# Kernel tuning notes

Measured on AMD Instinct MI355X. Metric: run time of the kernel, lower is better.

## Reference

```python
import jax, jax.numpy as jnp
import numpy as np

N_HEAD = 16
D_QK = 128
D_V = 128
D_MODEL = 2048
BATCH = 2
SEQ = 2048


def alibi_slopes(n_head):
    # standard ALiBi slopes: 2^(-8*i/n_head) for i = 1..n_head
    return jnp.asarray(2.0 ** (-8.0 * np.arange(1, n_head + 1) / n_head), dtype=jnp.float32)


def setup_inputs() -> dict:
    key = jax.random.key(0)
    k1, k2, k3, k4, k5 = jax.random.split(key, 5)
    x = jax.random.normal(k1, (BATCH, SEQ, D_MODEL), dtype=jnp.float32)
    # causal attention mask (1 = keep, 0 = masked), broadcast over heads
    causal = jnp.tril(jnp.ones((SEQ, SEQ), dtype=bool))
    attention_mask = jnp.broadcast_to(causal, (BATCH, 1, SEQ, SEQ))
    Wq = jax.random.normal(k2, (D_MODEL, N_HEAD * D_QK), dtype=jnp.float32) * (D_MODEL ** -0.5)
    Wk = jax.random.normal(k3, (D_MODEL, N_HEAD * D_QK), dtype=jnp.float32) * (D_MODEL ** -0.5)
    Wv = jax.random.normal(k4, (D_MODEL, N_HEAD * D_V), dtype=jnp.float32) * (D_MODEL ** -0.5)
    Wo = jax.random.normal(k5, (N_HEAD * D_V, D_MODEL), dtype=jnp.float32) * ((N_HEAD * D_V) ** -0.5)
    return {"x": x, "attention_mask": attention_mask, "Wq": Wq, "Wk": Wk, "Wv": Wv, "Wo": Wo}


def reference(x, attention_mask, Wq, Wk, Wv, Wo):
    B, S, _ = x.shape
    scale = D_QK ** -0.5
    q = (x @ Wq).reshape(B, S, N_HEAD, D_QK).transpose(0, 2, 1, 3)  # [B,H,S,dqk]
    k = (x @ Wk).reshape(B, S, N_HEAD, D_QK).transpose(0, 2, 1, 3)
    v = (x @ Wv).reshape(B, S, N_HEAD, D_V).transpose(0, 2, 1, 3)
    scores = jnp.einsum('bhid,bhjd->bhij', q, k) * scale  # [B,H,S,S]
    # ALiBi bias: slope_h * (j - i), negative penalty for distant past keys
    pos = jnp.arange(S, dtype=jnp.float32)
    rel = pos[None, :] - pos[:, None]  # [S,S]
    slopes = alibi_slopes(N_HEAD)
    scores = scores + slopes[None, :, None, None] * rel[None, None, :, :]
    scores = jnp.where(attention_mask, scores, jnp.float32(-jnp.inf))
    attn = jax.nn.softmax(scores, axis=-1)
    out = jnp.einsum('bhij,bhjd->bhid', attn, v)  # [B,H,S,dv]
    out = out.transpose(0, 2, 1, 3).reshape(B, S, N_HEAD * D_V)
    return out @ Wo
```

## Files before the change

### kernel.cpp

```cpp
#include <hip/hip_runtime.h>
#include <cstdint>

typedef unsigned short u16;
typedef __attribute__((ext_vector_type(4))) u16 u16x4;
typedef __attribute__((ext_vector_type(8))) u16 u16x8;
typedef __attribute__((ext_vector_type(8))) __bf16 bf16x8;
typedef __attribute__((ext_vector_type(4))) float f32x4;

#define LOG2E 1.44269504088896340736f

static __device__ __forceinline__ u16 f2bf(float f) {
  unsigned u = __builtin_bit_cast(unsigned, f);
  u += 0x7fffu + ((u >> 16) & 1u);
  return (u16)(u >> 16);
}
static __device__ __forceinline__ float bf2f(u16 v) {
  unsigned u = ((unsigned)v) << 16;
  return __builtin_bit_cast(float, u);
}

static __device__ __forceinline__ void gload16(const u16* g, u16* l) {
  __builtin_amdgcn_global_load_lds(
      (__attribute__((address_space(1))) void*)(uintptr_t)g,
      (__attribute__((address_space(3))) void*)(uintptr_t)l, 16, 0, 0);
}

static __device__ __forceinline__ bf16x8 lds_bf8(const void* p) {
  return __builtin_bit_cast(bf16x8, *(const u16x8*)p);
}

__global__ __launch_bounds__(256) void cast_x_kernel(const float* __restrict__ src,
                                                     u16* __restrict__ dst) {
  int i = (blockIdx.x * 256 + threadIdx.x) * 4;
  float4 v = *(const float4*)(src + i);
  u16x4 r = {f2bf(v.x), f2bf(v.y), f2bf(v.z), f2bf(v.w)};
  *(u16x4*)(dst + i) = r;
}

__device__ __forceinline__ void transpose_body(const float* __restrict__ src,
                                               u16* __restrict__ dst) {
  __shared__ float tile[32][33];
  const int n0 = blockIdx.x * 32, k0 = blockIdx.y * 32;
  const int tx = threadIdx.x & 31, ty = threadIdx.x >> 5;
#pragma unroll
  for (int r = 0; r < 4; ++r) {
    int row = r * 8 + ty;
    tile[row][tx] = src[(size_t)(k0 + row) * 2048 + n0 + tx];
  }
  __syncthreads();
#pragma unroll
  for (int r = 0; r < 4; ++r) {
    int row = r * 8 + ty;
    dst[(size_t)(n0 + row) * 2048 + k0 + tx] = f2bf(tile[tx][row]);
  }
}

__global__ __launch_bounds__(256) void transpose_w_kernel(const float* __restrict__ src,
                                                          u16* __restrict__ dst) {
  transpose_body(src, dst);
}

__global__ __launch_bounds__(256) void transpose_w3_kernel(const float* Wq, const float* Wk,
                                                           const float* Wv, u16* Wqt, u16* Wkt,
                                                           u16* Wvt) {
  const float* src = blockIdx.z == 0 ? Wq : (blockIdx.z == 1 ? Wk : Wv);
  u16* dst = blockIdx.z == 0 ? Wqt : (blockIdx.z == 1 ? Wkt : Wvt);
  transpose_body(src, dst);
}

#define GSTAGE(TILE, KH, BUF)                                                        \
  do {                                                                               \
    const int bk = (TILE) * 64 + (KH) * 32;                                          \
    u16* as_ = &lds[((BUF) * 2 + (KH)) * 8192];                                      \
    u16* bs_ = &lds[32768 + ((BUF) * 2 + (KH)) * BSLOT];                             \
    gload16(&A[(size_t)(m0 + sr) * 2048 + bk + scu], as_ + tid * 8);                 \
    gload16(&A[(size_t)(m0 + 128 + sr) * 2048 + bk + scu], as_ + 4096 + tid * 8);    \
    gload16(&Bt[(size_t)(n0 + sr) * 2048 + bk + scu], bs_ + tid * 8);                \
    if constexpr (BN == 256)                                                         \
      gload16(&Bt[(size_t)(n0 + 128 + sr) * 2048 + bk + scu], bs_ + 4096 + tid * 8); \
  } while (0)

#define GPH(BUF, KH, STAGE_STMT, VMLIT)                                              \
  do {                                                                               \
    const u16* as_ = &lds[((BUF) * 2 + (KH)) * 8192];                                \
    const u16* bs_ = &lds[32768 + ((BUF) * 2 + (KH)) * BSLOT];                       \
    bf16x8 af[8], bq[NF];                                                            \
    _Pragma("unroll") for (int mf = 0; mf < 8; ++mf) {                               \
      const int ar = wm * 128 + mf * 16 + l16;                                       \
      af[mf] = lds_bf8(&as_[(ar * 32 + lg * 8) ^ xsw]);                              \
    }                                                                                \
    _Pragma("unroll") for (int nf = 0; nf < NF; ++nf) {                              \
      const int br = wn * (BN / 4) + nf * 16 + l16;                                  \
      bq[nf] = lds_bf8(&bs_[(br * 32 + lg * 8) ^ xsw]);                              \
    }                                                                                \
    STAGE_STMT;                                                                      \
    asm volatile("s_barrier" ::: "memory");                                          \
    __builtin_amdgcn_s_setprio(1);                                                   \
    _Pragma("unroll") for (int mf = 0; mf < 8; ++mf)                                 \
        _Pragma("unroll") for (int nf = 0; nf < NF; ++nf) acc[mf][nf] =              \
            __builtin_amdgcn_mfma_f32_16x16x32_bf16(af[mf], bq[nf], acc[mf][nf], 0, 0, 0); \
    __builtin_amdgcn_s_setprio(0);                                                   \
    __builtin_amdgcn_sched_barrier(0);                                               \
    asm volatile("s_waitcnt vmcnt(" #VMLIT ")\n\ts_barrier" ::: "memory");           \
  } while (0)

template <int BN, int MODE>
__device__ __forceinline__ void gemm_dp(const u16* __restrict__ A, const u16* __restrict__ Bt,
                                        void* __restrict__ Cout, int m0, int n0) {
  constexpr int BSLOT = BN * 32;
  constexpr int NF = BN / 64;
  __shared__ u16 lds[32768 + 4 * BSLOT];
  const int tid = threadIdx.x, lane = tid & 63, w = tid >> 6;
  const int wm = w >> 2, wn = w & 3;
  const int l16 = lane & 15, lg = lane >> 4;
  const int sr = tid >> 2;
  const int scu = (((tid & 3) ^ ((tid >> 2) & 3))) * 8;
  const int xsw = (l16 & 3) * 8;

  f32x4 acc[8][NF];
#pragma unroll
  for (int i = 0; i < 8; ++i)
#pragma unroll
    for (int j = 0; j < NF; ++j) acc[i][j] = f32x4{0.f, 0.f, 0.f, 0.f};

  GSTAGE(0, 0, 0);
  GSTAGE(0, 1, 0);
  GSTAGE(1, 0, 1);
  if constexpr (BN == 256) {
    asm volatile("s_waitcnt vmcnt(8)\n\ts_barrier" ::: "memory");
    for (int m2 = 0; m2 < 30; m2 += 2) {
      GPH(0, 0, GSTAGE(m2 + 1, 1, 1), 8);
      GPH(0, 1, GSTAGE(m2 + 2, 0, 0), 8);
      GPH(1, 0, GSTAGE(m2 + 2, 1, 0), 8);
      GPH(1, 1, GSTAGE(m2 + 3, 0, 1), 8);
    }
    GPH(0, 0, GSTAGE(31, 1, 1), 8);
    GPH(0, 1, (void)0, 4);
    GPH(1, 0, (void)0, 0);
    GPH(1, 1, (void)0, 0);
  } else {
    asm volatile("s_waitcnt vmcnt(6)\n\ts_barrier" ::: "memory");
    for (int m2 = 0; m2 < 30; m2 += 2) {
      GPH(0, 0, GSTAGE(m2 + 1, 1, 1), 6);
      GPH(0, 1, GSTAGE(m2 + 2, 0, 0), 6);
      GPH(1, 0, GSTAGE(m2 + 2, 1, 0), 6);
      GPH(1, 1, GSTAGE(m2 + 3, 0, 1), 6);
    }
    GPH(0, 0, GSTAGE(31, 1, 1), 6);
    GPH(0, 1, (void)0, 3);
    GPH(1, 0, (void)0, 0);
    GPH(1, 1, (void)0, 0);
  }

  constexpr int WNS = BN / 4;
#pragma unroll
  for (int mf = 0; mf < 8; ++mf)
#pragma unroll
    for (int nf = 0; nf < NF; ++nf)
#pragma unroll
      for (int r = 0; r < 4; ++r) {
        const int row = m0 + wm * 128 + mf * 16 + lg * 4 + r;
        const int col = n0 + wn * WNS + nf * 16 + l16;
        const float v = acc[mf][nf][r];
        if constexpr (MODE == 0) {
          size_t off =
              (((size_t)(row >> 11) * 16 + (col >> 7)) * 2048 + (row & 2047)) * 128 + (col & 127);
          ((u16*)Cout)[off] = f2bf(v);
        } else if constexpr (MODE == 2) {
          size_t off =
              (((size_t)(col >> 11) * 16 + (row >> 7)) * 128 + (row & 127)) * 2048 + (col & 2047);
          ((u16*)Cout)[off] = f2bf(v);
        } else {
          ((float*)Cout)[(size_t)row * 2048 + col] = v;
        }
      }
}

__global__ __launch_bounds__(512, 2) void qkproj_kernel(const u16* xb, const u16* Wqt,
                                                        const u16* Wkt, u16* Qb, u16* Kb) {
  const int n0g = blockIdx.y * 256;
  const u16* Bt = (n0g < 2048) ? Wqt : Wkt;
  u16* dst = (n0g < 2048) ? Qb : Kb;
  gemm_dp<256, 0>(xb, Bt, dst, blockIdx.x * 256, n0g & 2047);
}

__global__ __launch_bounds__(512, 2) void vt_kernel(const u16* Wvt, const u16* xb, u16* Vb) {
  gemm_dp<128, 2>(Wvt, xb, Vb, blockIdx.x * 256, blockIdx.y * 128);
}

__global__ __launch_bounds__(512, 2) void out_kernel(const u16* OA, const u16* Wot, float* C) {
  gemm_dp<128, 1>(OA, Wot, C, blockIdx.x * 256, blockIdx.y * 128);
}

__global__ __launch_bounds__(256) void attn_kernel(const u16* __restrict__ Q,
                                                   const u16* __restrict__ Kg,
                                                   const u16* __restrict__ Vg,
                                                   u16* __restrict__ O,
                                                   u16* __restrict__ Opart,
                                                   float* __restrict__ Lp) {
  const int tid = threadIdx.x, lane = tid & 63, w = tid >> 6;
  const int l16 = lane & 15, lg = lane >> 4;

  const int bid = blockIdx.x;
  const int bh = bid / 23, u = bid - bh * 23;
  int tile, st0, st1, slot = 0;
  bool multi;
  if (u < 14) {
    multi = true;
    const int ti = u >> 1, ch = u & 1;
    tile = 9 + ti;
    const int s = 2 * tile + 2;
    st0 = ch * 18;
    st1 = min(st0 + 18, s);
    slot = bh * 14 + u;
  } else {
    multi = false;
    tile = 22 - u;
    st0 = 0;
    st1 = 2 * tile + 2;
  }
  const int q0 = tile * 128;
  const int h = bh & 15, b = bh >> 4;
  const float sl2 = exp2f(-0.5f * (float)(h + 1)) * LOG2E;
  const float sc2 = 0.08838834764831845f * LOG2E;

  __shared__ u16 Kl[64 * 128];
  __shared__ u16 Vl[128 * 64];
  __shared__ u16 Pl[128 * 64];

  const size_t qk_base = (size_t)bh * 2048 * 128;
  const size_t v_base = (size_t)bh * 128 * 2048;

  bf16x8 qf[2][4];
#pragma unroll
  for (int mf = 0; mf < 2; ++mf)
#pragma unroll
    for (int ks = 0; ks < 4; ++ks)
      qf[mf][ks] =
          lds_bf8(&Q[qk_base + (size_t)(q0 + w * 32 + mf * 16 + l16) * 128 + ks * 32 + lg * 8]);

  f32x4 oacc[2][8];
#pragma unroll
  for (int i = 0; i < 2; ++i)
#pragma unroll
    for (int j = 0; j < 8; ++j) oacc[i][j] = f32x4{0.f, 0.f, 0.f, 0.f};
  float lsum[2][2];
  lsum[0][0] = lsum[0][1] = lsum[1][0] = lsum[1][1] = 0.f;

  float ab[2][4][4];
#pragma unroll
  for (int mf = 0; mf < 2; ++mf)
#pragma unroll
    for (int nf = 0; nf < 4; ++nf)
#pragma unroll
      for (int r = 0; r < 4; ++r)
        ab[mf][nf][r] =
            (float)(st0 * 64 + nf * 16 + lg * 4 + r - q0 - w * 32 - mf * 16 - l16) * sl2;
  const float abinc = 64.0f * sl2;

  const u16* kgp = Kg + qk_base + (size_t)(tid >> 4) * 128 + (tid & 15) * 8;
  const u16* vgp = Vg + v_base + (size_t)(tid >> 3) * 2048 + (tid & 7) * 8;
  const int kwo = ((tid >> 4) * 256 + (tid & 15) * 16) ^ (((tid >> 4) & 7) << 4);
  const int vwo = ((tid >> 3) * 128 + (tid & 7) * 16) ^ (((tid >> 3) & 7) << 4);

  u16x8 kr[4], vr[4];
#define LOADREGS(STX)                                                        \
  do {                                                                       \
    const size_t ko = (size_t)(STX)*8192, vo = (size_t)(STX)*64;             \
    _Pragma("unroll") for (int s = 0; s < 4; ++s) {                          \
      kr[s] = *(const u16x8*)(kgp + ko + s * 2048);                          \
      vr[s] = *(const u16x8*)(vgp + vo + s * 65536);                         \
    }                                                                        \
  } while (0)

#define WRITEBUF()                                                           \
  do {                                                                       \
    _Pragma("unroll") for (int s = 0; s < 4; ++s) {                          \
      *(u16x8*)((char*)Kl + s * 4096 + kwo) = kr[s];                         \
      *(u16x8*)((char*)Vl + s * 4096 + vwo) = vr[s];                         \
    }                                                                        \
  } while (0)

#define ASTEP(MASKED)                                                                     \
  do {                                                                                    \
    if (st + 1 < st1) LOADREGS(st + 1);                                                   \
    f32x4 sacc[2][4];                                                                     \
    _Pragma("unroll") for (int i = 0; i < 2; ++i)                                         \
        _Pragma("unroll") for (int j = 0; j < 4; ++j) sacc[i][j] = f32x4{0.f, 0.f, 0.f, 0.f}; \
    __builtin_amdgcn_s_setprio(1);                                                        \
    _Pragma("unroll") for (int ks = 0; ks < 4; ++ks) {                                    \
      bf16x8 kf[4];                                                                       \
      _Pragma("unroll") for (int nf = 0; nf < 4; ++nf) {                                  \
        int j = nf * 16 + l16;                                                            \
        kf[nf] = lds_bf8((char*)Kl + ((j * 256 + (ks * 32 + lg * 8) * 2) ^ ((j & 7) << 4))); \
      }                                                                                   \
      _Pragma("unroll") for (int mf = 0; mf < 2; ++mf)                                    \
          _Pragma("unroll") for (int nf = 0; nf < 4; ++nf) sacc[mf][nf] =                 \
              __builtin_amdgcn_mfma_f32_16x16x32_bf16(kf[nf], qf[mf][ks], sacc[mf][nf], 0, 0, 0); \
    }                                                                                     \
    __builtin_amdgcn_s_setprio(0);                                                        \
    _Pragma("unroll") for (int mf = 0; mf < 2; ++mf)                                      \
        _Pragma("unroll") for (int nf = 0; nf < 4; ++nf) {                                \
      float pvv[4];                                                                       \
      _Pragma("unroll") for (int r = 0; r < 4; ++r) {                                     \
        float s2 = fmaf(sacc[mf][nf][r], sc2, ab[mf][nf][r]);                             \
        float pv = exp2f(s2);                                                             \
        if (MASKED) {                                                                     \
          const int rel = st * 64 + nf * 16 + lg * 4 + r - q0 - w * 32 - mf * 16 - l16;   \
          pv = (rel <= 0) ? pv : 0.f;                                                     \
        }                                                                                 \
        pvv[r] = pv;                                                                      \
        ab[mf][nf][r] += abinc;                                                           \
      }                                                                                   \
      lsum[mf][nf & 1] += (pvv[0] + pvv[1]) + (pvv[2] + pvv[3]);                          \
      unsigned w0_, w1_;                                                                  \
      asm("v_cvt_pk_bf16_f32 %0, %1, %2" : "=v"(w0_) : "v"(pvv[0]), "v"(pvv[1]));         \
      asm("v_cvt_pk_bf16_f32 %0, %1, %2" : "=v"(w1_) : "v"(pvv[2]), "v"(pvv[3]));         \
      const int qrow = w * 32 + mf * 16 + l16;                                            \
      uint2 pw_{w0_, w1_};                                                                \
      *(uint2*)((char*)Pl + ((qrow * 128 + (nf * 16 + lg * 4) * 2) ^ ((qrow & 7) << 4))) = pw_; \
    }                                                                                     \
    __builtin_amdgcn_s_setprio(1);                                                        \
    _Pragma("unroll") for (int ks = 0; ks < 2; ++ks) {                                    \
      bf16x8 pf[2];                                                                       \
      _Pragma("unroll") for (int mf = 0; mf < 2; ++mf) {                                  \
        int qrow = w * 32 + mf * 16 + l16;                                                \
        pf[mf] = lds_bf8((char*)Pl + ((qrow * 128 + (ks * 32 + lg * 8) * 2) ^ ((qrow & 7) << 4))); \
      }                                                                                   \
      _Pragma("unroll") for (int nf = 0; nf < 8; ++nf) {                                  \
        int d = nf * 16 + l16;                                                            \
        bf16x8 vf =                                                                       \
            lds_bf8((char*)Vl + ((d * 128 + (ks * 32 + lg * 8) * 2) ^ ((d & 7) << 4)));   \
        _Pragma("unroll") for (int mf = 0; mf < 2; ++mf) oacc[mf][nf] =                   \
            __builtin_amdgcn_mfma_f32_16x16x32_bf16(pf[mf], vf, oacc[mf][nf], 0, 0, 0);   \
      }                                                                                   \
    }                                                                                     \
    __builtin_amdgcn_s_setprio(0);                                                        \
    if (st + 1 < st1) {                                                                   \
      __syncthreads();                                                                    \
      WRITEBUF();                                                                         \
      __syncthreads();                                                                    \
    }                                                                                     \
  } while (0)

  LOADREGS(st0);
  WRITEBUF();
  __syncthreads();

  const int dstart = (multi && (u & 1) == 0) ? st1 : st1 - 2;
  int st = st0;
  for (; st < dstart; ++st) ASTEP(false);
  for (; st < st1; ++st) ASTEP(true);
#undef LOADREGS
#undef WRITEBUF
#undef ASTEP

  float lr[2];
#pragma unroll
  for (int mf = 0; mf < 2; ++mf) {
    float v = lsum[mf][0] + lsum[mf][1];
    v += __shfl_xor(v, 16, 64);
    v += __shfl_xor(v, 32, 64);
    lr[mf] = v;
  }

  if (multi) {
    if (lg == 0) {
#pragma unroll
      for (int mf = 0; mf < 2; ++mf) Lp[(size_t)slot * 128 + w * 32 + mf * 16 + l16] = lr[mf];
    }
#pragma unroll
    for (int mf = 0; mf < 2; ++mf)
#pragma unroll
      for (int r = 0; r < 4; ++r) {
        const int row = w * 32 + mf * 16 + lg * 4 + r;
#pragma unroll
        for (int nf = 0; nf < 8; ++nf) {
          int col = nf * 16 + l16;
          Opart[((size_t)slot * 128 + row) * 128 + col] = f2bf(oacc[mf][nf][r]);
        }
      }
  } else {
#pragma unroll
    for (int mf = 0; mf < 2; ++mf)
#pragma unroll
      for (int r = 0; r < 4; ++r) {
        const float lv = __shfl(lr[mf], lg * 4 + r, 64);
        const float inv = 1.0f / lv;
        const int srow = q0 + w * 32 + mf * 16 + lg * 4 + r;
#pragma unroll
        for (int nf = 0; nf < 8; ++nf) {
          int col = h * 128 + nf * 16 + l16;
          O[((size_t)b * 2048 + srow) * 2048 + col] = f2bf(oacc[mf][nf][r] * inv);
        }
      }
  }
}

__global__ __launch_bounds__(256) void combine_kernel(const u16* __restrict__ Opart,
                                                      const float* __restrict__ Lp,
                                                      u16* __restrict__ O) {
  const int bx = blockIdx.x;
  const int bh = bx / 7, ti = bx % 7;
  const int tile = 9 + ti;
  const int slot0 = bh * 14 + ti * 2, slot1 = slot0 + 1;
  const int b = bh >> 4, h = bh & 15;
  const int q0 = tile * 128;
  const int tid = threadIdx.x;
  const int colg = (tid & 15) * 8, rowb = tid >> 4;
#pragma unroll
  for (int rr = 0; rr < 8; ++rr) {
    const int row = rowb + rr * 16;
    const float l0 = Lp[(size_t)slot0 * 128 + row];
    const float l1 = Lp[(size_t)slot1 * 128 + row];
    const float inv = 1.0f / (l0 + l1);
    u16x8 p0 = *(const u16x8*)&Opart[((size_t)slot0 * 128 + row) * 128 + colg];
    u16x8 p1 = *(const u16x8*)&Opart[((size_t)slot1 * 128 + row) * 128 + colg];
    u16x8 o;
#pragma unroll
    for (int e = 0; e < 8; ++e) o[e] = f2bf((bf2f(p0[e]) + bf2f(p1[e])) * inv);
    *(u16x8*)&O[((size_t)b * 2048 + q0 + row) * 2048 + h * 128 + colg] = o;
  }
}

extern "C" void kernel_launch(void* const* d_in, const int* in_sizes, int n_in, void* d_out,
                              int out_size, void* d_ws, size_t ws_size, hipStream_t stream) {
  const float* x = (const float*)d_in[0];
  const float* Wq = (const float*)d_in[2];
  const float* Wk = (const float*)d_in[3];
  const float* Wv = (const float*)d_in[4];
  const float* Wo = (const float*)d_in[5];
  char* ws = (char*)d_ws;

  const size_t MB = 1048576;
  u16* xb = (u16*)(ws);
  u16* Qb = (u16*)(ws + 16 * MB);
  u16* Kb = (u16*)(ws + 32 * MB);
  u16* Vb = (u16*)(ws + 48 * MB);
  u16* Wqt = (u16*)(ws + 64 * MB);
  u16* Wkt = (u16*)(ws + 72 * MB);
  u16* Wvt = (u16*)(ws + 80 * MB);
  u16* Wot = Wqt;
  u16* OA = xb;
  u16* Opart = (u16*)(ws + 72 * MB);
  float* Lpf = (float*)(ws + 72 * MB + 448ull * 128 * 128 * 2);

  cast_x_kernel<<<8192, 256, 0, stream>>>(x, xb);
  transpose_w3_kernel<<<dim3(64, 64, 3), 256, 0, stream>>>(Wq, Wk, Wv, Wqt, Wkt, Wvt);
  qkproj_kernel<<<dim3(16, 16), 512, 0, stream>>>(xb, Wqt, Wkt, Qb, Kb);
  vt_kernel<<<dim3(8, 32), 512, 0, stream>>>(Wvt, xb, Vb);
  transpose_w_kernel<<<dim3(64, 64), 256, 0, stream>>>(Wo, Wot);
  attn_kernel<<<dim3(736), 256, 0, stream>>>(Qb, Kb, Vb, OA, Opart, Lpf);
  combine_kernel<<<dim3(224), 256, 0, stream>>>(Opart, Lpf, OA);
  out_kernel<<<dim3(16, 16), 512, 0, stream>>>(OA, Wot, (float*)d_out);
}
```

Measured before the change: 282.6 us.

## Halve attention query tile to 64 rows and stage K/V via direct global-to-LDS loads

```diff
diff --git a/kernel.cpp b/kernel.cpp
--- a/kernel.cpp
+++ b/kernel.cpp
@@ -201,92 +201,73 @@
   const int tid = threadIdx.x, lane = tid & 63, w = tid >> 6;
   const int l16 = lane & 15, lg = lane >> 4;
 
-  const int bid = blockIdx.x;
-  const int bh = bid / 23, u = bid - bh * 23;
+  const int u = blockIdx.x >> 5, bh = blockIdx.x & 31;
   int tile, st0, st1, slot = 0;
-  bool multi;
-  if (u < 14) {
+  bool multi = false;
+  if (u == 0) { tile = 17; st0 = 0; st1 = 18; }
+  else if (u == 1) { tile = 16; st0 = 0; st1 = 17; }
+  else if (u < 30) {
     multi = true;
-    const int ti = u >> 1, ch = u & 1;
-    tile = 9 + ti;
-    const int s = 2 * tile + 2;
-    st0 = ch * 18;
-    st1 = min(st0 + 18, s);
-    slot = bh * 14 + u;
-  } else {
-    multi = false;
-    tile = 22 - u;
-    st0 = 0;
-    st1 = 2 * tile + 2;
-  }
-  const int q0 = tile * 128;
+    const int c = u - 2, ti = c >> 1, ch = c & 1;
+    tile = 31 - ti;
+    const int s = tile + 1, half = (s + 1) >> 1;
+    st0 = ch ? half : 0;
+    st1 = ch ? s : half;
+    slot = bh * 28 + c;
+  } else { tile = 45 - u; st0 = 0; st1 = tile + 1; }
+
+  const int q0 = tile * 64;
   const int h = bh & 15, b = bh >> 4;
   const float sl2 = exp2f(-0.5f * (float)(h + 1)) * LOG2E;
   const float sc2 = 0.08838834764831845f * LOG2E;
 
   __shared__ u16 Kl[64 * 128];
   __shared__ u16 Vl[128 * 64];
-  __shared__ u16 Pl[128 * 64];
+  __shared__ u16 Pl[64 * 64];
 
   const size_t qk_base = (size_t)bh * 2048 * 128;
   const size_t v_base = (size_t)bh * 128 * 2048;
 
-  bf16x8 qf[2][4];
-#pragma unroll
-  for (int mf = 0; mf < 2; ++mf)
-#pragma unroll
-    for (int ks = 0; ks < 4; ++ks)
-      qf[mf][ks] =
-          lds_bf8(&Q[qk_base + (size_t)(q0 + w * 32 + mf * 16 + l16) * 128 + ks * 32 + lg * 8]);
-
-  f32x4 oacc[2][8];
-#pragma unroll
-  for (int i = 0; i < 2; ++i)
-#pragma unroll
-    for (int j = 0; j < 8; ++j) oacc[i][j] = f32x4{0.f, 0.f, 0.f, 0.f};
-  float lsum[2][2];
-  lsum[0][0] = lsum[0][1] = lsum[1][0] = lsum[1][1] = 0.f;
-
-  float ab[2][4][4];
-#pragma unroll
-  for (int mf = 0; mf < 2; ++mf)
-#pragma unroll
-    for (int nf = 0; nf < 4; ++nf)
-#pragma unroll
-      for (int r = 0; r < 4; ++r)
-        ab[mf][nf][r] =
-            (float)(st0 * 64 + nf * 16 + lg * 4 + r - q0 - w * 32 - mf * 16 - l16) * sl2;
+  const u16* kgs = Kg + qk_base + (size_t)(tid >> 4) * 128 + (((tid & 15) ^ ((tid >> 4) & 7)) * 8);
+  const u16* vgs = Vg + v_base + (size_t)(tid >> 3) * 2048 + (((tid & 7) ^ ((tid >> 3) & 7)) * 8);
+
+#define STAGEKV(STX)                                                        \
+  do {                                                                      \
+    const int j0s = (STX)*64;                                               \
+    _Pragma("unroll") for (int s = 0; s < 4; ++s) {                         \
+      gload16(kgs + (size_t)(j0s + s * 16) * 128, Kl + s * 2048 + tid * 8); \
+      gload16(vgs + (size_t)s * 32 * 2048 + j0s, Vl + s * 2048 + tid * 8);  \
+    }                                                                       \
+  } while (0)
+
+  STAGEKV(st0);
+
+  bf16x8 qf[4];
+#pragma unroll
+  for (int ks = 0; ks < 4; ++ks)
+    qf[ks] = lds_bf8(&Q[qk_base + (size_t)(q0 + w * 16 + l16) * 128 + ks * 32 + lg * 8]);
+
+  f32x4 oacc[8];
+#pragma unroll
+  for (int j = 0; j < 8; ++j) oacc[j] = f32x4{0.f, 0.f, 0.f, 0.f};
+  float lsum0 = 0.f, lsum1 = 0.f;
+
+  float ab4[4], rsl[4];
+#pragma unroll
+  for (int nf = 0; nf < 4; ++nf)
+    ab4[nf] = (float)(st0 * 64 + nf * 16 - q0 - w * 16 - l16) * sl2;
+#pragma unroll
+  for (int r = 0; r < 4; ++r) rsl[r] = (float)(lg * 4 + r) * sl2;
   const float abinc = 64.0f * sl2;
-
-  const u16* kgp = Kg + qk_base + (size_t)(tid >> 4) * 128 + (tid & 15) * 8;
-  const u16* vgp = Vg + v_base + (size_t)(tid >> 3) * 2048 + (tid & 7) * 8;
-  const int kwo = ((tid >> 4) * 256 + (tid & 15) * 16) ^ (((tid >> 4) & 7) << 4);
-  const int vwo = ((tid >> 3) * 128 + (tid & 7) * 16) ^ (((tid >> 3) & 7) << 4);
-
-  u16x8 kr[4], vr[4];
-#define LOADREGS(STX)                                                        \
-  do {                                                                       \
-    const size_t ko = (size_t)(STX)*8192, vo = (size_t)(STX)*64;             \
-    _Pragma("unroll") for (int s = 0; s < 4; ++s) {                          \
-      kr[s] = *(const u16x8*)(kgp + ko + s * 2048);                          \
-      vr[s] = *(const u16x8*)(vgp + vo + s * 65536);                         \
-    }                                                                        \
-  } while (0)
-
-#define WRITEBUF()                                                           \
-  do {                                                                       \
-    _Pragma("unroll") for (int s = 0; s < 4; ++s) {                          \
-      *(u16x8*)((char*)Kl + s * 4096 + kwo) = kr[s];                         \
-      *(u16x8*)((char*)Vl + s * 4096 + vwo) = vr[s];                         \
-    }                                                                        \
-  } while (0)
+  const int qrow = w * 16 + l16;
+  const int dmaskb = lg * 4 - w * 16 - l16;
+
+  __syncthreads();
 
 #define ASTEP(MASKED)                                                                     \
   do {                                                                                    \
-    if (st + 1 < st1) LOADREGS(st + 1);                                                   \
-    f32x4 sacc[2][4];                                                                     \
-    _Pragma("unroll") for (int i = 0; i < 2; ++i)                                         \
-        _Pragma("unroll") for (int j = 0; j < 4; ++j) sacc[i][j] = f32x4{0.f, 0.f, 0.f, 0.f}; \
+    f32x4 sacc[4];                                                                        \
+    _Pragma("unroll") for (int j = 0; j < 4; ++j) sacc[j] = f32x4{0.f, 0.f, 0.f, 0.f};    \
     __builtin_amdgcn_s_setprio(1);                                                        \
     _Pragma("unroll") for (int ks = 0; ks < 4; ++ks) {                                    \
       bf16x8 kf[4];                                                                       \
@@ -294,106 +275,75 @@
         int j = nf * 16 + l16;                                                            \
         kf[nf] = lds_bf8((char*)Kl + ((j * 256 + (ks * 32 + lg * 8) * 2) ^ ((j & 7) << 4))); \
       }                                                                                   \
-      _Pragma("unroll") for (int mf = 0; mf < 2; ++mf)                                    \
-          _Pragma("unroll") for (int nf = 0; nf < 4; ++nf) sacc[mf][nf] =                 \
-              __builtin_amdgcn_mfma_f32_16x16x32_bf16(kf[nf], qf[mf][ks], sacc[mf][nf], 0, 0, 0); \
+      _Pragma("unroll") for (int nf = 0; nf < 4; ++nf) sacc[nf] =                         \
+          __builtin_amdgcn_mfma_f32_16x16x32_bf16(kf[nf], qf[ks], sacc[nf], 0, 0, 0);     \
     }                                                                                     \
     __builtin_amdgcn_s_setprio(0);                                                        \
-    _Pragma("unroll") for (int mf = 0; mf < 2; ++mf)                                      \
-        _Pragma("unroll") for (int nf = 0; nf < 4; ++nf) {                                \
+    _Pragma("unroll") for (int nf = 0; nf < 4; ++nf) {                                    \
       float pvv[4];                                                                       \
       _Pragma("unroll") for (int r = 0; r < 4; ++r) {                                     \
-        float s2 = fmaf(sacc[mf][nf][r], sc2, ab[mf][nf][r]);                             \
+        float s2 = fmaf(sacc[nf][r], sc2, ab4[nf] + rsl[r]);                              \
         float pv = exp2f(s2);                                                             \
-        if (MASKED) {                                                                     \
-          const int rel = st * 64 + nf * 16 + lg * 4 + r - q0 - w * 32 - mf * 16 - l16;   \
-          pv = (rel <= 0) ? pv : 0.f;                                                     \
-        }                                                                                 \
+        if (MASKED) pv = (nf * 16 + r + dmaskb <= 0) ? pv : 0.f;                          \
         pvv[r] = pv;                                                                      \
-        ab[mf][nf][r] += abinc;                                                           \
       }                                                                                   \
-      lsum[mf][nf & 1] += (pvv[0] + pvv[1]) + (pvv[2] + pvv[3]);                          \
+      ab4[nf] += abinc;                                                                   \
+      lsum0 += pvv[0] + pvv[1];                                                           \
+      lsum1 += pvv[2] + pvv[3];                                                           \
       unsigned w0_, w1_;                                                                  \
       asm("v_cvt_pk_bf16_f32 %0, %1, %2" : "=v"(w0_) : "v"(pvv[0]), "v"(pvv[1]));         \
       asm("v_cvt_pk_bf16_f32 %0, %1, %2" : "=v"(w1_) : "v"(pvv[2]), "v"(pvv[3]));         \
-      const int qrow = w * 32 + mf * 16 + l16;                                            \
       uint2 pw_{w0_, w1_};                                                                \
       *(uint2*)((char*)Pl + ((qrow * 128 + (nf * 16 + lg * 4) * 2) ^ ((qrow & 7) << 4))) = pw_; \
     }                                                                                     \
     __builtin_amdgcn_s_setprio(1);                                                        \
     _Pragma("unroll") for (int ks = 0; ks < 2; ++ks) {                                    \
-      bf16x8 pf[2];                                                                       \
-      _Pragma("unroll") for (int mf = 0; mf < 2; ++mf) {                                  \
-        int qrow = w * 32 + mf * 16 + l16;                                                \
-        pf[mf] = lds_bf8((char*)Pl + ((qrow * 128 + (ks * 32 + lg * 8) * 2) ^ ((qrow & 7) << 4))); \
-      }                                                                                   \
+      bf16x8 pf =                                                                         \
+          lds_bf8((char*)Pl + ((qrow * 128 + (ks * 32 + lg * 8) * 2) ^ ((qrow & 7) << 4))); \
       _Pragma("unroll") for (int nf = 0; nf < 8; ++nf) {                                  \
         int d = nf * 16 + l16;                                                            \
         bf16x8 vf =                                                                       \
             lds_bf8((char*)Vl + ((d * 128 + (ks * 32 + lg * 8) * 2) ^ ((d & 7) << 4)));   \
-        _Pragma("unroll") for (int mf = 0; mf < 2; ++mf) oacc[mf][nf] =                   \
-            __builtin_amdgcn_mfma_f32_16x16x32_bf16(pf[mf], vf, oacc[mf][nf], 0, 0, 0);   \
+        oacc[nf] = __builtin_amdgcn_mfma_f32_16x16x32_bf16(pf, vf, oacc[nf], 0, 0, 0);    \
       }                                                                                   \
     }                                                                                     \
     __builtin_amdgcn_s_setprio(0);                                                        \
     if (st + 1 < st1) {                                                                   \
       __syncthreads();                                                                    \
-      WRITEBUF();                                                                         \
+      STAGEKV(st + 1);                                                                    \
       __syncthreads();                                                                    \
     }                                                                                     \
   } while (0)
 
-  LOADREGS(st0);
-  WRITEBUF();
-  __syncthreads();
-
-  const int dstart = (multi && (u & 1) == 0) ? st1 : st1 - 2;
   int st = st0;
-  for (; st < dstart; ++st) ASTEP(false);
+  const int bulk_end = min(st1, tile);
+  for (; st < bulk_end; ++st) ASTEP(false);
   for (; st < st1; ++st) ASTEP(true);
-#undef LOADREGS
-#undef WRITEBUF
+#undef STAGEKV
 #undef ASTEP
 
-  float lr[2];
-#pragma unroll
-  for (int mf = 0; mf < 2; ++mf) {
-    float v = lsum[mf][0] + lsum[mf][1];
-    v += __shfl_xor(v, 16, 64);
-    v += __shfl_xor(v, 32, 64);
-    lr[mf] = v;
-  }
+  float lr = lsum0 + lsum1;
+  lr += __shfl_xor(lr, 16, 64);
+  lr += __shfl_xor(lr, 32, 64);
 
   if (multi) {
-    if (lg == 0) {
-#pragma unroll
-      for (int mf = 0; mf < 2; ++mf) Lp[(size_t)slot * 128 + w * 32 + mf * 16 + l16] = lr[mf];
+    if (lg == 0) Lp[(size_t)slot * 64 + qrow] = lr;
+#pragma unroll
+    for (int r = 0; r < 4; ++r) {
+      const int row = w * 16 + lg * 4 + r;
+#pragma unroll
+      for (int nf = 0; nf < 8; ++nf)
+        Opart[((size_t)slot * 64 + row) * 128 + nf * 16 + l16] = f2bf(oacc[nf][r]);
     }
-#pragma unroll
-    for (int mf = 0; mf < 2; ++mf)
-#pragma unroll
-      for (int r = 0; r < 4; ++r) {
-        const int row = w * 32 + mf * 16 + lg * 4 + r;
-#pragma unroll
-        for (int nf = 0; nf < 8; ++nf) {
-          int col = nf * 16 + l16;
-          Opart[((size_t)slot * 128 + row) * 128 + col] = f2bf(oacc[mf][nf][r]);
-        }
-      }
   } else {
 #pragma unroll
-    for (int mf = 0; mf < 2; ++mf)
-#pragma unroll
-      for (int r = 0; r < 4; ++r) {
-        const float lv = __shfl(lr[mf], lg * 4 + r, 64);
-        const float inv = 1.0f / lv;
-        const int srow = q0 + w * 32 + mf * 16 + lg * 4 + r;
-#pragma unroll
-        for (int nf = 0; nf < 8; ++nf) {
-          int col = h * 128 + nf * 16 + l16;
-          O[((size_t)b * 2048 + srow) * 2048 + col] = f2bf(oacc[mf][nf][r] * inv);
-        }
-      }
+    for (int r = 0; r < 4; ++r) {
+      const float inv = 1.0f / __shfl(lr, lg * 4 + r, 64);
+      const int srow = q0 + w * 16 + lg * 4 + r;
+#pragma unroll
+      for (int nf = 0; nf < 8; ++nf)
+        O[((size_t)b * 2048 + srow) * 2048 + h * 128 + nf * 16 + l16] = f2bf(oacc[nf][r] * inv);
+    }
   }
 }
 
@@ -401,21 +351,21 @@
                                                       const float* __restrict__ Lp,
                                                       u16* __restrict__ O) {
   const int bx = blockIdx.x;
-  const int bh = bx / 7, ti = bx % 7;
-  const int tile = 9 + ti;
-  const int slot0 = bh * 14 + ti * 2, slot1 = slot0 + 1;
+  const int bh = bx / 14, ti = bx % 14;
+  const int tile = 31 - ti;
+  const int slot0 = bh * 28 + ti * 2, slot1 = slot0 + 1;
   const int b = bh >> 4, h = bh & 15;
-  const int q0 = tile * 128;
+  const int q0 = tile * 64;
   const int tid = threadIdx.x;
   const int colg = (tid & 15) * 8, rowb = tid >> 4;
 #pragma unroll
-  for (int rr = 0; rr < 8; ++rr) {
+  for (int rr = 0; rr < 4; ++rr) {
     const int row = rowb + rr * 16;
-    const float l0 = Lp[(size_t)slot0 * 128 + row];
-    const float l1 = Lp[(size_t)slot1 * 128 + row];
+    const float l0 = Lp[(size_t)slot0 * 64 + row];
+    const float l1 = Lp[(size_t)slot1 * 64 + row];
     const float inv = 1.0f / (l0 + l1);
-    u16x8 p0 = *(const u16x8*)&Opart[((size_t)slot0 * 128 + row) * 128 + colg];
-    u16x8 p1 = *(const u16x8*)&Opart[((size_t)slot1 * 128 + row) * 128 + colg];
+    u16x8 p0 = *(const u16x8*)&Opart[((size_t)slot0 * 64 + row) * 128 + colg];
+    u16x8 p1 = *(const u16x8*)&Opart[((size_t)slot1 * 64 + row) * 128 + colg];
     u16x8 o;
 #pragma unroll
     for (int e = 0; e < 8; ++e) o[e] = f2bf((bf2f(p0[e]) + bf2f(p1[e])) * inv);
@@ -443,14 +393,14 @@
   u16* Wot = Wqt;
   u16* OA = xb;
   u16* Opart = (u16*)(ws + 72 * MB);
-  float* Lpf = (float*)(ws + 72 * MB + 448ull * 128 * 128 * 2);
+  float* Lpf = (float*)(ws + 72 * MB + 896ull * 64 * 128 * 2);
 
   cast_x_kernel<<<8192, 256, 0, stream>>>(x, xb);
   transpose_w3_kernel<<<dim3(64, 64, 3), 256, 0, stream>>>(Wq, Wk, Wv, Wqt, Wkt, Wvt);
   qkproj_kernel<<<dim3(16, 16), 512, 0, stream>>>(xb, Wqt, Wkt, Qb, Kb);
   vt_kernel<<<dim3(8, 32), 512, 0, stream>>>(Wvt, xb, Vb);
   transpose_w_kernel<<<dim3(64, 64), 256, 0, stream>>>(Wo, Wot);
-  attn_kernel<<<dim3(736), 256, 0, stream>>>(Qb, Kb, Vb, OA, Opart, Lpf);
-  combine_kernel<<<dim3(224), 256, 0, stream>>>(Opart, Lpf, OA);
+  attn_kernel<<<dim3(1472), 256, 0, stream>>>(Qb, Kb, Vb, OA, Opart, Lpf);
+  combine_kernel<<<dim3(448), 256, 0, stream>>>(Opart, Lpf, OA);
   out_kernel<<<dim3(16, 16), 512, 0, stream>>>(OA, Wot, (float*)d_out);
 }
```

After: 252.1 us. -10.8%, faster.
